# Kernel optimization log

Measured on AMD Instinct MI355X. Metric: run time of the kernel, lower is better.

## Reference

```python
import jax, jax.numpy as jnp
import numpy as np

N_NODES = 20000
N_EDGES = 640000
D = 128          # vision_dim == topo_dim
OUT = 256        # out_dim
B = 64           # image batch == num graphs
HW = 64
NEG_SLOPE = 0.2


def _sn(w2d, u):
    """PyTorch spectral_norm forward: one power iteration (u,v detached), W/sigma."""
    v = jax.lax.stop_gradient(w2d.T @ u)
    v = v / (jnp.linalg.norm(v) + 1e-12)
    u2 = jax.lax.stop_gradient(w2d @ v)
    u2 = u2 / (jnp.linalg.norm(u2) + 1e-12)
    sigma = u2 @ (w2d @ v)
    return w2d / sigma


def _leaky(x):
    return jnp.where(x >= 0, x, NEG_SLOPE * x)


def setup_inputs() -> dict:
    key = jax.random.key(0)
    ks = jax.random.split(key, 16)
    vis = jax.random.normal(ks[0], (B, D, HW, HW), dtype=jnp.float32)
    topo = jax.random.normal(ks[1], (N_NODES, D), dtype=jnp.float32)
    edge_index = jax.random.randint(ks[2], (2, N_EDGES), 0, N_NODES, dtype=jnp.int64)
    batch = jnp.sort(jax.random.randint(ks[3], (N_NODES,), 0, B, dtype=jnp.int64))
    s = 0.05
    conv_w = jax.random.normal(ks[4], (D, D, 3, 3), dtype=jnp.float32) * s
    conv_b = jnp.zeros((D,), dtype=jnp.float32)
    conv_u = jax.random.normal(ks[5], (D,), dtype=jnp.float32)
    fcv_w = jax.random.normal(ks[6], (OUT, D * 4), dtype=jnp.float32) * s
    fcv_b = jnp.zeros((OUT,), dtype=jnp.float32)
    fcv_u = jax.random.normal(ks[7], (OUT,), dtype=jnp.float32)
    gcn_w = jax.random.normal(ks[8], (D, D), dtype=jnp.float32) * s
    gcn_b = jnp.zeros((D,), dtype=jnp.float32)
    fct_w = jax.random.normal(ks[9], (OUT, D), dtype=jnp.float32) * s
    fct_b = jnp.zeros((OUT,), dtype=jnp.float32)
    fct_u = jax.random.normal(ks[10], (OUT,), dtype=jnp.float32)
    return dict(vis=vis, topo=topo, edge_index=edge_index, batch=batch,
                conv_w=conv_w, conv_b=conv_b, conv_u=conv_u,
                fcv_w=fcv_w, fcv_b=fcv_b, fcv_u=fcv_u,
                gcn_w=gcn_w, gcn_b=gcn_b,
                fct_w=fct_w, fct_b=fct_b, fct_u=fct_u)


def reference(vis, topo, edge_index, batch,
              conv_w, conv_b, conv_u,
              fcv_w, fcv_b, fcv_u,
              gcn_w, gcn_b,
              fct_w, fct_b, fct_u):
    # ---- vision head: spectral-norm conv3x3 -> leaky_relu -> adaptive max pool 2x2 -> SN linear
    cw = _sn(conv_w.reshape(D, -1), conv_u).reshape(conv_w.shape)
    x = jax.lax.conv_general_dilated(vis, cw, window_strides=(1, 1), padding='VALID',
                                     dimension_numbers=('NCHW', 'OIHW', 'NCHW'))
    x = _leaky(x + conv_b[None, :, None, None])              # [B, D, 62, 62]
    Bc, C, H, W = x.shape
    x = x.reshape(Bc, C, 2, H // 2, 2, W // 2).max(axis=(3, 5))  # adaptive max pool -> [B,D,2,2]
    x = x.reshape(Bc, -1)                                    # [B, 4D]
    vis_score = x @ _sn(fcv_w, fcv_u).T + fcv_b              # [B, OUT]

    # ---- topo head: GCNConv (sym-norm, self-loops) -> leaky_relu -> global max pool -> SN linear
    n = topo.shape[0]
    loop = jnp.arange(n, dtype=edge_index.dtype)
    src = jnp.concatenate([edge_index[0], loop])
    dst = jnp.concatenate([edge_index[1], loop])
    deg = jax.ops.segment_sum(jnp.ones_like(dst, dtype=topo.dtype), dst, num_segments=n)
    dis = jnp.where(deg > 0, jax.lax.rsqrt(jnp.maximum(deg, 1.0)), 0.0)
    norm = dis[src] * dis[dst]                               # [E+N]
    xw = topo @ gcn_w                                        # [N, D]
    h = jax.ops.segment_sum(norm[:, None] * xw[src], dst, num_segments=n) + gcn_b
    h = _leaky(h)
    pooled = jax.ops.segment_max(h, batch, num_segments=B)   # [B, D]
    topo_score = pooled @ _sn(fct_w, fct_u).T + fct_b        # [B, OUT]

    return (vis_score, topo_score)
```

## Files before the change

### kernel.cpp

```cpp
#include <hip/hip_runtime.h>
#include <hip/hip_bf16.h>
#include <float.h>
#include <stdint.h>

#define NB   64
#define CD   128
#define OUTD 256
#define NNODE 20000
#define NEDGE 640000

typedef __bf16 bf16x8 __attribute__((ext_vector_type(8)));
typedef __bf16 bf16x4 __attribute__((ext_vector_type(4)));
typedef float  f32x4  __attribute__((ext_vector_type(4)));

__device__ inline void gl_lds16(const void* g, void* l) {
  __builtin_amdgcn_global_load_lds(
      (const __attribute__((address_space(1))) void*)g,
      (__attribute__((address_space(3))) void*)l, 16, 0, 0);
}

__device__ inline void atomicMaxF(float* addr, float val) {
  if (val >= 0.f) atomicMax((int*)addr, __float_as_int(val));
  else            atomicMin((unsigned int*)addr, __float_as_uint(val));
}

__global__ void k_init(float* __restrict__ pooled_v, float* __restrict__ pooled_t,
                       int* __restrict__ cnt, int* __restrict__ fill,
                       float* __restrict__ sn_scratch, int* __restrict__ ntotal) {
  const int i = blockIdx.x * 256 + threadIdx.x;
  if (i < NB * CD * 4) pooled_v[i] = -FLT_MAX;
  if (i < NB * CD)     pooled_t[i] = -FLT_MAX;
  if (i < NNODE)       { cnt[i] = 0; fill[i] = 0; }
  if (i < 1796)        sn_scratch[i] = 0.0f;
  if (i == 0)          *ntotal = 0;
}

__global__ __launch_bounds__(256) void k_sn_v(const float* __restrict__ conv_w, const float* __restrict__ conv_u,
                                              const float* __restrict__ fcv_w,  const float* __restrict__ fcv_u,
                                              const float* __restrict__ fct_w,  const float* __restrict__ fct_u,
                                              float* __restrict__ sn) {
  const int bb = blockIdx.x;
  const float* W; const float* u; float* v; int C; int r0;
  if (bb < 16)      { W = conv_w; u = conv_u; v = sn;        C = 1152; r0 = bb * 8; }
  else if (bb < 48) { W = fcv_w;  u = fcv_u;  v = sn + 1152; C = 512;  r0 = (bb - 16) * 8; }
  else              { W = fct_w;  u = fct_u;  v = sn + 1664; C = 128;  r0 = (bb - 48) * 8; }
  const int tid = threadIdx.x;
  float acc[5] = {0.f, 0.f, 0.f, 0.f, 0.f};
  for (int i = r0; i < r0 + 8; ++i) {
    const float ui = u[i];
    const float* row = W + (size_t)i * C;
    #pragma unroll
    for (int t = 0; t < 5; ++t) {
      const int j = tid + t * 256;
      if (j < C) acc[t] += ui * row[j];
    }
  }
  #pragma unroll
  for (int t = 0; t < 5; ++t) {
    const int j = tid + t * 256;
    if (j < C) atomicAdd(&v[j], acc[t]);
  }
}

__global__ __launch_bounds__(256) void k_sn_w(const float* __restrict__ conv_w,
                                              const float* __restrict__ fcv_w,
                                              const float* __restrict__ fct_w,
                                              float* __restrict__ sn) {
  const int gw = blockIdx.x * 4 + (threadIdx.x >> 6);
  const int lane = threadIdx.x & 63;
  const float* W; const float* v; int C, m, row;
  if (gw < 128)      { W = conv_w; v = sn;        C = 1152; m = 0; row = gw; }
  else if (gw < 384) { W = fcv_w;  v = sn + 1152; C = 512;  m = 1; row = gw - 128; }
  else               { W = fct_w;  v = sn + 1664; C = 128;  m = 2; row = gw - 384; }
  const float* wr = W + (size_t)row * C;
  float y = 0.f;
  for (int c = lane; c < C; c += 64) y += wr[c] * v[c];
  #pragma unroll
  for (int s = 32; s > 0; s >>= 1) y += __shfl_xor(y, s, 64);
  if (lane == 0) atomicAdd(&sn[1792 + m], y * y);
}

__global__ __launch_bounds__(256) void k_sn_fin(const float* __restrict__ sn, float* __restrict__ inv_sigma) {
  __shared__ float red[256];
  const int tid = threadIdx.x;
  const int off[4] = {0, 1152, 1664, 1792};
  for (int m = 0; m < 3; ++m) {
    const int C = off[m + 1] - off[m];
    float ss = 0.f;
    for (int j = tid; j < C; j += 256) { const float a = sn[off[m] + j]; ss += a * a; }
    red[tid] = ss; __syncthreads();
    for (int s = 128; s > 0; s >>= 1) { if (tid < s) red[tid] += red[tid + s]; __syncthreads(); }
    if (tid == 0) inv_sigma[m] = (sqrtf(red[0]) + 1e-12f) / sqrtf(sn[1792 + m]);
    __syncthreads();
  }
}

__global__ __launch_bounds__(256, 4) void k_prep(const float* __restrict__ vis, __bf16* __restrict__ visT2,
                                                 const float* __restrict__ conv_w, const float* __restrict__ inv_sigma,
                                                 __hip_bfloat16* __restrict__ Bt2,
                                                 const int* __restrict__ dst, int* __restrict__ cnt) {
  __shared__ __bf16 tile[16384];
  const int bid = blockIdx.x;
  const int t = threadIdx.x;
  if (bid < 1024) {
    const int b = bid >> 4, y0 = (bid & 15) << 2;
    const int wave = t >> 6, lane = t & 63;
    const float* src = vis + (size_t)b * 524288 + y0 * 64 + lane * 4;
    #pragma unroll
    for (int ph = 0; ph < 2; ++ph) {
      #pragma unroll
      for (int i = 0; i < 16; ++i) {
        const int cl = wave * 16 + i;
        const int c = (ph << 6) + cl;
        const f32x4 v = *(const f32x4*)(src + (size_t)c * 4096);
        bf16x4 o;
        #pragma unroll
        for (int k = 0; k < 4; ++k) o[k] = (__bf16)v[k];
        *(bf16x4*)&tile[cl * 256 + lane * 4] = o;
      }
      __syncthreads();
      #pragma unroll
      for (int yy = 0; yy < 4; ++yy) {
        bf16x8* dstv = (bf16x8*)(visT2 + ((size_t)((b << 6) + y0 + yy) << 13)) + (ph << 9);
        #pragma unroll
        for (int k = 0; k < 2; ++k) {
          const int j = k * 256 + t;
          const int gl = j >> 6, x = j & 63;
          union { bf16x8 v; __bf16 h[8]; } u;
          #pragma unroll
          for (int cc = 0; cc < 8; ++cc)
            u.h[cc] = tile[(gl * 8 + cc) * 256 + yy * 64 + x];
          dstv[j] = u.v;
        }
      }
      if (ph == 0) __syncthreads();
    }
  } else if (bid < 1600) {
    const int tt = (bid - 1024) * 256 + t;
    if (tt < 147456) {
      const int j = tt & 7, n = (tt >> 3) & 127, s = (tt >> 10) & 7, hk = (tt >> 13) & 1, tap = tt >> 14;
      const int ci = hk * 64 + s * 8 + j;
      Bt2[tt] = __float2bfloat16(conv_w[n * 1152 + ci * 9 + tap] * inv_sigma[0]);
    }
  } else {
    const int e = (bid - 1600) * 256 + t;
    if (e < NEDGE) atomicAdd(&cnt[dst[e]], 1);
  }
}

__global__ __launch_bounds__(256, 4) void k_conv(const __hip_bfloat16* __restrict__ visT2,
                                                 const __hip_bfloat16* __restrict__ Bt2,
                                                 const float* __restrict__ conv_b,
                                                 float* __restrict__ pooled_v, int b0) {
  __shared__ bf16x8 lds_a[1024];
  __shared__ bf16x8 lds_b[1024];
  const int bx = blockIdx.x;
  const int b = b0 + bx / 31;
  const int y0 = (bx % 31) * 2;
  const int tid = threadIdx.x;
  const int wave = tid >> 6, lane = tid & 63;
  const int quad = lane >> 4, l15 = lane & 15;

  f32x4 acc[8][2];
  #pragma unroll
  for (int i = 0; i < 8; ++i) {
    acc[i][0] = f32x4{0.f, 0.f, 0.f, 0.f};
    acc[i][1] = f32x4{0.f, 0.f, 0.f, 0.f};
  }

  const __hip_bfloat16* vb = visT2 + ((size_t)b << 19);
  const int s0 = wave << 1;
  bf16x8* ldsA0 = &lds_a[s0 << 7];
  bf16x8* ldsB0 = &lds_b[s0 << 7];
  const int lane8 = lane << 3;

  for (int ky = 0; ky < 3; ++ky) {
    for (int kx = 0; kx < 3; ++kx) {
      const int tap = ky * 3 + kx;
      #pragma unroll
      for (int hk = 0; hk < 2; ++hk) {
        const __hip_bfloat16* a0p = vb + ((size_t)(((y0 + ky) << 4) + (hk << 3) + s0) << 9) + (kx << 3) + lane8;
        const __hip_bfloat16* a1p = vb + ((size_t)(((y0 + 1 + ky) << 4) + (hk << 3) + s0) << 9) + (kx << 3) + lane8;
        const __hip_bfloat16* bp  = Bt2 + (((size_t)(((tap << 1) + hk) << 3) + s0) << 10) + lane8;
        gl_lds16(a0p,        ldsA0);
        gl_lds16(a1p,        ldsA0 + 64);
        gl_lds16(a0p + 512,  ldsA0 + 128);
        gl_lds16(a1p + 512,  ldsA0 + 192);
        gl_lds16(bp,         ldsB0);
        gl_lds16(bp + 512,   ldsB0 + 64);
        gl_lds16(bp + 1024,  ldsB0 + 128);
        gl_lds16(bp + 1536,  ldsB0 + 192);
        __syncthreads();
        const bf16x8 b00 = lds_b[(quad << 7) + (wave << 5) + l15];
        const bf16x8 b01 = lds_b[(quad << 7) + (wave << 5) + 16 + l15];
        const bf16x8 b10 = lds_b[((4 + quad) << 7) + (wave << 5) + l15];
        const bf16x8 b11 = lds_b[((4 + quad) << 7) + (wave << 5) + 16 + l15];
        #pragma unroll
        for (int mt = 0; mt < 8; ++mt) {
          const bf16x8 a0 = lds_a[(quad << 7) + (mt << 4) + l15];
          const bf16x8 a1 = lds_a[((4 + quad) << 7) + (mt << 4) + l15];
          acc[mt][0] = __builtin_amdgcn_mfma_f32_16x16x32_bf16(a0, b00, acc[mt][0], 0, 0, 0);
          acc[mt][1] = __builtin_amdgcn_mfma_f32_16x16x32_bf16(a0, b01, acc[mt][1], 0, 0, 0);
          acc[mt][0] = __builtin_amdgcn_mfma_f32_16x16x32_bf16(a1, b10, acc[mt][0], 0, 0, 0);
          acc[mt][1] = __builtin_amdgcn_mfma_f32_16x16x32_bf16(a1, b11, acc[mt][1], 0, 0, 0);
        }
        __syncthreads();
      }
    }
  }

  const float cb0 = conv_b[(wave << 5) + l15];
  const float cb1 = conv_b[(wave << 5) + 16 + l15];
  float pmax[2][2][2];
  #pragma unroll
  for (int i = 0; i < 8; ++i) (&pmax[0][0][0])[i] = -FLT_MAX;

  #pragma unroll
  for (int mt = 0; mt < 8; ++mt) {
    const int py = (y0 + (mt >> 2)) >= 31 ? 1 : 0;
    #pragma unroll
    for (int r = 0; r < 4; ++r) {
      const int x = ((mt & 3) << 4) + (quad << 2) + r;
      if (x < 62) {
        const int px = x >= 31 ? 1 : 0;
        float v0 = acc[mt][0][r] + cb0;  v0 = v0 >= 0.f ? v0 : 0.2f * v0;
        float v1 = acc[mt][1][r] + cb1;  v1 = v1 >= 0.f ? v1 : 0.2f * v1;
        pmax[0][py][px] = fmaxf(pmax[0][py][px], v0);
        pmax[1][py][px] = fmaxf(pmax[1][py][px], v1);
      }
    }
  }
  #pragma unroll
  for (int nt = 0; nt < 2; ++nt)
    #pragma unroll
    for (int py = 0; py < 2; ++py)
      #pragma unroll
      for (int px = 0; px < 2; ++px) {
        float v = pmax[nt][py][px];
        v = fmaxf(v, __shfl_xor(v, 16, 64));
        v = fmaxf(v, __shfl_xor(v, 32, 64));
        if (quad == 0) {
          const int n = (wave << 5) + (nt << 4) + l15;
          atomicMaxF(&pooled_v[(size_t)b * 512 + n * 4 + py * 2 + px], v);
        }
      }
}

__global__ __launch_bounds__(256) void k_scan_xw(const int* __restrict__ cnt, int* __restrict__ offset,
                                                 int* __restrict__ total, float* __restrict__ dis,
                                                 const float* __restrict__ topo, const float* __restrict__ gcn_w,
                                                 __bf16* __restrict__ xws) {
  __shared__ f32x4 w4[4096];
  __shared__ int sbase;
  const int tid = threadIdx.x;
  if (blockIdx.x < 79) {
    int* red = (int*)w4;
    const int n = blockIdx.x * 256 + tid;
    const int v = (n < NNODE) ? cnt[n] : 0;
    red[tid] = v; __syncthreads();
    for (int d = 1; d < 256; d <<= 1) {
      const int t = (tid >= d) ? red[tid - d] : 0;
      __syncthreads();
      red[tid] += t;
      __syncthreads();
    }
    if (tid == 255) sbase = atomicAdd(total, red[255]);
    __syncthreads();
    if (n < NNODE) {
      offset[n] = sbase + red[tid] - v;
      dis[n] = rsqrtf((float)(v + 1));
    }
  } else {
    const f32x4* gw4 = (const f32x4*)gcn_w;
    for (int i = tid; i < 4096; i += 256) w4[i] = gw4[i];
    __syncthreads();
    const int n0 = (blockIdx.x - 79) * 64;
    const int jq = tid & 31, ns = tid >> 5;
    for (int pass = 0; pass < 8; ++pass) {
      const int n = n0 + pass * 8 + ns;
      if (n >= NNODE) break;
      const f32x4* tr4 = (const f32x4*)(topo + (size_t)n * 128);
      f32x4 a = {0.f, 0.f, 0.f, 0.f};
      for (int d4 = 0; d4 < 32; ++d4) {
        const f32x4 t = tr4[d4];
        const int base = (d4 << 7) + jq;
        #pragma unroll
        for (int m = 0; m < 4; ++m) {
          const f32x4 w = w4[base + m * 32];
          #pragma unroll
          for (int k = 0; k < 4; ++k) a[k] += t[m] * w[k];
        }
      }
      const float dn = rsqrtf((float)(cnt[n] + 1));
      bf16x4 o;
      #pragma unroll
      for (int k = 0; k < 4; ++k) o[k] = (__bf16)(a[k] * dn);
      ((bf16x4*)xws)[(size_t)n * 32 + jq] = o;
    }
  }
}

__global__ void k_bucket(const int* __restrict__ src, const int* __restrict__ dst,
                         const int* __restrict__ offset, int* __restrict__ fill,
                         int* __restrict__ sorted_src) {
  const int e = blockIdx.x * 256 + threadIdx.x;
  if (e >= NEDGE) return;
  const int t = dst[e];
  const int pos = atomicAdd(&fill[t], 1);
  sorted_src[offset[t] + pos] = src[e];
}

__global__ __launch_bounds__(256) void k_gather(const int* __restrict__ sorted_src,
                                                const int* __restrict__ offset, const int* __restrict__ cnt,
                                                const float* __restrict__ dis, const __bf16* __restrict__ xws,
                                                const float* __restrict__ gcn_b, const int* __restrict__ batch,
                                                float* __restrict__ pooled_t) {
  __shared__ float hred[4][128];
  __shared__ int hg[4];
  const int wave = threadIdx.x >> 6, lane = threadIdx.x & 63;
  const int n = blockIdx.x * 4 + wave;
  const int slot = lane >> 4, l16 = lane & 15;
  const int e0 = offset[n], ne = cnt[n];
  const bf16x8* x8 = (const bf16x8*)xws;
  float a[8];
  if (slot == 0) {
    const bf16x8 v = x8[(size_t)n * 16 + l16];
    #pragma unroll
    for (int k = 0; k < 8; ++k) a[k] = (float)v[k];
  } else {
    #pragma unroll
    for (int k = 0; k < 8; ++k) a[k] = 0.f;
  }
  for (int e = slot; e < ne; e += 4) {
    const int s = sorted_src[e0 + e];
    const bf16x8 v = x8[(size_t)s * 16 + l16];
    #pragma unroll
    for (int k = 0; k < 8; ++k) a[k] += (float)v[k];
  }
  #pragma unroll
  for (int k = 0; k < 8; ++k) {
    a[k] += __shfl_xor(a[k], 16, 64);
    a[k] += __shfl_xor(a[k], 32, 64);
  }
  if (lane == 0) hg[wave] = batch[n];
  if (slot == 0) {
    const float dn = dis[n];
    #pragma unroll
    for (int k = 0; k < 8; ++k) {
      float t = gcn_b[(l16 << 3) + k] + dn * a[k];
      hred[wave][(l16 << 3) + k] = t >= 0.f ? t : 0.2f * t;
    }
  }
  __syncthreads();
  const int tid = threadIdx.x;
  if (tid < 128) {
    const int g0 = hg[0], g1 = hg[1], g2 = hg[2], g3 = hg[3];
    if (g0 == g1 && g1 == g2 && g2 == g3) {
      const float m = fmaxf(fmaxf(hred[0][tid], hred[1][tid]), fmaxf(hred[2][tid], hred[3][tid]));
      atomicMaxF(&pooled_t[g0 * 128 + tid], m);
    } else {
      atomicMaxF(&pooled_t[g0 * 128 + tid], hred[0][tid]);
      atomicMaxF(&pooled_t[g1 * 128 + tid], hred[1][tid]);
      atomicMaxF(&pooled_t[g2 * 128 + tid], hred[2][tid]);
      atomicMaxF(&pooled_t[g3 * 128 + tid], hred[3][tid]);
    }
  }
}

__global__ __launch_bounds__(256) void k_fc(const float* __restrict__ pooled_v, const float* __restrict__ fcv_w,
                                            const float* __restrict__ fcv_b,
                                            const float* __restrict__ pooled_t, const float* __restrict__ fct_w,
                                            const float* __restrict__ fct_b,
                                            const float* __restrict__ inv_sigma, float* __restrict__ out) {
  const int tid = threadIdx.x;
  if (blockIdx.x < 64) {
    __shared__ f32x4 xr[128];
    const int b = blockIdx.x;
    if (tid < 128) xr[tid] = ((const f32x4*)pooled_v)[b * 128 + tid];
    __syncthreads();
    const f32x4* wr = (const f32x4*)(fcv_w + (size_t)tid * 512);
    f32x4 a4 = {0.f, 0.f, 0.f, 0.f};
    for (int f = 0; f < 128; ++f) {
      const f32x4 x = xr[f];
      const f32x4 w = wr[f];
      #pragma unroll
      for (int k = 0; k < 4; ++k) a4[k] += x[k] * w[k];
    }
    const float a = a4[0] + a4[1] + a4[2] + a4[3];
    out[b * 256 + tid] = a * inv_sigma[1] + fcv_b[tid];
  } else {
    __shared__ f32x4 xr2[32];
    const int b = blockIdx.x - 64;
    if (tid < 32) xr2[tid] = ((const f32x4*)pooled_t)[b * 32 + tid];
    __syncthreads();
    const f32x4* wr = (const f32x4*)(fct_w + (size_t)tid * 128);
    f32x4 a4 = {0.f, 0.f, 0.f, 0.f};
    for (int f = 0; f < 32; ++f) {
      const f32x4 x = xr2[f];
      const f32x4 w = wr[f];
      #pragma unroll
      for (int k = 0; k < 4; ++k) a4[k] += x[k] * w[k];
    }
    const float a = a4[0] + a4[1] + a4[2] + a4[3];
    out[NB * 256 + b * 256 + tid] = a * inv_sigma[2] + fct_b[tid];
  }
}

extern "C" void kernel_launch(void* const* d_in, const int* in_sizes, int n_in,
                              void* d_out, int out_size, void* d_ws, size_t ws_size,
                              hipStream_t stream) {
  const float* vis    = (const float*)d_in[0];
  const float* topo   = (const float*)d_in[1];
  const int*   eidx   = (const int*)d_in[2];
  const int*   batch  = (const int*)d_in[3];
  const float* conv_w = (const float*)d_in[4];
  const float* conv_b = (const float*)d_in[5];
  const float* conv_u = (const float*)d_in[6];
  const float* fcv_w  = (const float*)d_in[7];
  const float* fcv_b  = (const float*)d_in[8];
  const float* fcv_u  = (const float*)d_in[9];
  const float* gcn_w  = (const float*)d_in[10];
  const float* gcn_b  = (const float*)d_in[11];
  const float* fct_w  = (const float*)d_in[12];
  const float* fct_b  = (const float*)d_in[13];
  const float* fct_u  = (const float*)d_in[14];
  float* out = (float*)d_out;

  char* p = (char*)d_ws;
  float* inv_sigma  = (float*)p; p += 256;
  float* sn_scratch = (float*)p; p += 1796 * 4 + 240;
  float* pooled_v   = (float*)p; p += (size_t)NB * 512 * 4;
  float* pooled_t   = (float*)p; p += (size_t)NB * 128 * 4;
  int*   cnt        = (int*)p;   p += (size_t)NNODE * 4;
  int*   offset     = (int*)p;   p += (size_t)NNODE * 4;
  int*   fill       = (int*)p;   p += (size_t)NNODE * 4;
  float* dis        = (float*)p; p += (size_t)NNODE * 4;
  int*   ntotal     = (int*)p;   p += 256;
  int*   sorted_src = (int*)p;   p += (size_t)NEDGE * 4;
  __bf16* xws       = (__bf16*)p; p += (size_t)NNODE * 128 * 2 + 256;
  __hip_bfloat16* Bt2 = (__hip_bfloat16*)p; p += (size_t)147456 * 2;
  p = (char*)(((uintptr_t)p + 255) & ~(uintptr_t)255);
  __bf16* visT2 = (__bf16*)p;

  hipLaunchKernelGGL(k_init,    dim3(128),  dim3(256), 0, stream, pooled_v, pooled_t, cnt, fill, sn_scratch, ntotal);
  hipLaunchKernelGGL(k_sn_v,    dim3(80),   dim3(256), 0, stream, conv_w, conv_u, fcv_w, fcv_u, fct_w, fct_u, sn_scratch);
  hipLaunchKernelGGL(k_sn_w,    dim3(160),  dim3(256), 0, stream, conv_w, fcv_w, fct_w, sn_scratch);
  hipLaunchKernelGGL(k_sn_fin,  dim3(1),    dim3(256), 0, stream, sn_scratch, inv_sigma);
  hipLaunchKernelGGL(k_prep,    dim3(4100), dim3(256), 0, stream, vis, visT2, conv_w, inv_sigma, Bt2, eidx + NEDGE, cnt);
  hipLaunchKernelGGL(k_scan_xw, dim3(392),  dim3(256), 0, stream, cnt, offset, ntotal, dis, topo, gcn_w, xws);
  hipLaunchKernelGGL(k_conv,    dim3(32*31), dim3(256), 0, stream, (const __hip_bfloat16*)visT2, Bt2, conv_b, pooled_v, 0);
  hipLaunchKernelGGL(k_conv,    dim3(32*31), dim3(256), 0, stream, (const __hip_bfloat16*)visT2, Bt2, conv_b, pooled_v, 32);
  hipLaunchKernelGGL(k_bucket,  dim3(2500), dim3(256), 0, stream, eidx, eidx + NEDGE, offset, fill, sorted_src);
  hipLaunchKernelGGL(k_gather,  dim3(5000), dim3(256), 0, stream, sorted_src, offset, cnt, dis, xws, gcn_b, batch, pooled_t);
  hipLaunchKernelGGL(k_fc,      dim3(128),  dim3(256), 0, stream, pooled_v, fcv_w, fcv_b, pooled_t, fct_w, fct_b, inv_sigma, out);
}
```

Before: 485.1 us.

## Fuse launch chain into fewer multi-role kernels and merge conv launches

Reduces the launch sequence from eleven kernels to seven. Init, spectral-norm v computation and the vis transpose are merged into one front kernel. The sn row norms and the edge degree count share a kernel, and the sigma finalisation moves into the scan kernel. Weight packing is combined with edge bucketing, and the two conv launches are merged into one grid over all 64 images. Spectral-norm atomics are replaced by direct per-column and per-row writes to scratch. The aim is to cut launch gaps and serial tiny kernels, at the cost of more block-role branching and reordered dependencies between stages.

```diff
diff --git a/kernel.cpp b/kernel.cpp
--- a/kernel.cpp
+++ b/kernel.cpp
@@ -24,86 +24,39 @@
   else            atomicMin((unsigned int*)addr, __float_as_uint(val));
 }
 
-__global__ void k_init(float* __restrict__ pooled_v, float* __restrict__ pooled_t,
-                       int* __restrict__ cnt, int* __restrict__ fill,
-                       float* __restrict__ sn_scratch, int* __restrict__ ntotal) {
-  const int i = blockIdx.x * 256 + threadIdx.x;
-  if (i < NB * CD * 4) pooled_v[i] = -FLT_MAX;
-  if (i < NB * CD)     pooled_t[i] = -FLT_MAX;
-  if (i < NNODE)       { cnt[i] = 0; fill[i] = 0; }
-  if (i < 1796)        sn_scratch[i] = 0.0f;
-  if (i == 0)          *ntotal = 0;
-}
-
-__global__ __launch_bounds__(256) void k_sn_v(const float* __restrict__ conv_w, const float* __restrict__ conv_u,
-                                              const float* __restrict__ fcv_w,  const float* __restrict__ fcv_u,
-                                              const float* __restrict__ fct_w,  const float* __restrict__ fct_u,
-                                              float* __restrict__ sn) {
-  const int bb = blockIdx.x;
-  const float* W; const float* u; float* v; int C; int r0;
-  if (bb < 16)      { W = conv_w; u = conv_u; v = sn;        C = 1152; r0 = bb * 8; }
-  else if (bb < 48) { W = fcv_w;  u = fcv_u;  v = sn + 1152; C = 512;  r0 = (bb - 16) * 8; }
-  else              { W = fct_w;  u = fct_u;  v = sn + 1664; C = 128;  r0 = (bb - 48) * 8; }
-  const int tid = threadIdx.x;
-  float acc[5] = {0.f, 0.f, 0.f, 0.f, 0.f};
-  for (int i = r0; i < r0 + 8; ++i) {
-    const float ui = u[i];
-    const float* row = W + (size_t)i * C;
-    #pragma unroll
-    for (int t = 0; t < 5; ++t) {
-      const int j = tid + t * 256;
-      if (j < C) acc[t] += ui * row[j];
-    }
-  }
-  #pragma unroll
-  for (int t = 0; t < 5; ++t) {
-    const int j = tid + t * 256;
-    if (j < C) atomicAdd(&v[j], acc[t]);
-  }
-}
-
-__global__ __launch_bounds__(256) void k_sn_w(const float* __restrict__ conv_w,
-                                              const float* __restrict__ fcv_w,
-                                              const float* __restrict__ fct_w,
-                                              float* __restrict__ sn) {
-  const int gw = blockIdx.x * 4 + (threadIdx.x >> 6);
-  const int lane = threadIdx.x & 63;
-  const float* W; const float* v; int C, m, row;
-  if (gw < 128)      { W = conv_w; v = sn;        C = 1152; m = 0; row = gw; }
-  else if (gw < 384) { W = fcv_w;  v = sn + 1152; C = 512;  m = 1; row = gw - 128; }
-  else               { W = fct_w;  v = sn + 1664; C = 128;  m = 2; row = gw - 384; }
-  const float* wr = W + (size_t)row * C;
-  float y = 0.f;
-  for (int c = lane; c < C; c += 64) y += wr[c] * v[c];
-  #pragma unroll
-  for (int s = 32; s > 0; s >>= 1) y += __shfl_xor(y, s, 64);
-  if (lane == 0) atomicAdd(&sn[1792 + m], y * y);
-}
-
-__global__ __launch_bounds__(256) void k_sn_fin(const float* __restrict__ sn, float* __restrict__ inv_sigma) {
-  __shared__ float red[256];
-  const int tid = threadIdx.x;
-  const int off[4] = {0, 1152, 1664, 1792};
-  for (int m = 0; m < 3; ++m) {
-    const int C = off[m + 1] - off[m];
-    float ss = 0.f;
-    for (int j = tid; j < C; j += 256) { const float a = sn[off[m] + j]; ss += a * a; }
-    red[tid] = ss; __syncthreads();
-    for (int s = 128; s > 0; s >>= 1) { if (tid < s) red[tid] += red[tid + s]; __syncthreads(); }
-    if (tid == 0) inv_sigma[m] = (sqrtf(red[0]) + 1e-12f) / sqrtf(sn[1792 + m]);
-    __syncthreads();
-  }
-}
-
-__global__ __launch_bounds__(256, 4) void k_prep(const float* __restrict__ vis, __bf16* __restrict__ visT2,
-                                                 const float* __restrict__ conv_w, const float* __restrict__ inv_sigma,
-                                                 __hip_bfloat16* __restrict__ Bt2,
-                                                 const int* __restrict__ dst, int* __restrict__ cnt) {
+
+__global__ __launch_bounds__(256, 4) void k_front(float* __restrict__ pooled_v, float* __restrict__ pooled_t,
+                                                  int* __restrict__ cnt, int* __restrict__ fill,
+                                                  int* __restrict__ ntotal,
+                                                  const float* __restrict__ conv_w, const float* __restrict__ conv_u,
+                                                  const float* __restrict__ fcv_w,  const float* __restrict__ fcv_u,
+                                                  const float* __restrict__ fct_w,  const float* __restrict__ fct_u,
+                                                  float* __restrict__ sn,
+                                                  const float* __restrict__ vis, __bf16* __restrict__ visT2) {
   __shared__ __bf16 tile[16384];
   const int bid = blockIdx.x;
   const int t = threadIdx.x;
-  if (bid < 1024) {
-    const int b = bid >> 4, y0 = (bid & 15) << 2;
+  if (bid < 128) {
+    const int i = bid * 256 + t;
+    if (i < NB * CD * 4) pooled_v[i] = -FLT_MAX;
+    if (i < NB * CD)     pooled_t[i] = -FLT_MAX;
+    if (i < NNODE)       { cnt[i] = 0; fill[i] = 0; }
+    if (i == 0)          *ntotal = 0;
+  } else if (bid < 136) {
+    const int bb = bid - 128;
+    const float* W; const float* u; float* v; int C, R, c0;
+    if (bb < 5)      { W = conv_w; u = conv_u; v = sn;        C = 1152; R = 128; c0 = bb * 256; }
+    else if (bb < 7) { W = fcv_w;  u = fcv_u;  v = sn + 1152; C = 512;  R = 256; c0 = (bb - 5) * 256; }
+    else             { W = fct_w;  u = fct_u;  v = sn + 1664; C = 128;  R = 256; c0 = 0; }
+    const int col = c0 + t;
+    if (col < C) {
+      float acc = 0.f;
+      for (int i = 0; i < R; ++i) acc += u[i] * W[(size_t)i * C + col];
+      v[col] = acc;
+    }
+  } else {
+    const int bb = bid - 136;
+    const int b = bb >> 4, y0 = (bb & 15) << 2;
     const int wave = t >> 6, lane = t & 63;
     const float* src = vis + (size_t)b * 524288 + y0 * 64 + lane * 4;
     #pragma unroll
@@ -135,27 +88,139 @@
       }
       if (ph == 0) __syncthreads();
     }
-  } else if (bid < 1600) {
-    const int tt = (bid - 1024) * 256 + t;
-    if (tt < 147456) {
-      const int j = tt & 7, n = (tt >> 3) & 127, s = (tt >> 10) & 7, hk = (tt >> 13) & 1, tap = tt >> 14;
-      const int ci = hk * 64 + s * 8 + j;
-      Bt2[tt] = __float2bfloat16(conv_w[n * 1152 + ci * 9 + tap] * inv_sigma[0]);
-    }
-  } else {
-    const int e = (bid - 1600) * 256 + t;
-    if (e < NEDGE) atomicAdd(&cnt[dst[e]], 1);
+  }
+}
+
+__global__ __launch_bounds__(256) void k_mid(const float* __restrict__ conv_w,
+                                             const float* __restrict__ fcv_w,
+                                             const float* __restrict__ fct_w,
+                                             float* __restrict__ sn,
+                                             const int* __restrict__ dstE, int* __restrict__ cnt) {
+  const int bid = blockIdx.x;
+  if (bid < 160) {
+    const int gw = bid * 4 + (threadIdx.x >> 6);
+    const int lane = threadIdx.x & 63;
+    const float* W; const float* v; int C, row;
+    if (gw < 128)      { W = conv_w; v = sn;        C = 1152; row = gw; }
+    else if (gw < 384) { W = fcv_w;  v = sn + 1152; C = 512;  row = gw - 128; }
+    else               { W = fct_w;  v = sn + 1664; C = 128;  row = gw - 384; }
+    const float* wr = W + (size_t)row * C;
+    float y = 0.f;
+    for (int c = lane; c < C; c += 64) y += wr[c] * v[c];
+    #pragma unroll
+    for (int s = 32; s > 0; s >>= 1) y += __shfl_xor(y, s, 64);
+    if (lane == 0) sn[1800 + gw] = y * y;
+  } else {
+    const int e = (bid - 160) * 256 + threadIdx.x;
+    if (e < NEDGE) atomicAdd(&cnt[dstE[e]], 1);
+  }
+}
+
+__global__ __launch_bounds__(256) void k_scan_xw(const int* __restrict__ cnt, int* __restrict__ offset,
+                                                 int* __restrict__ total, float* __restrict__ dis,
+                                                 const float* __restrict__ topo, const float* __restrict__ gcn_w,
+                                                 __bf16* __restrict__ xws,
+                                                 float* __restrict__ sn, float* __restrict__ inv_sigma) {
+  __shared__ f32x4 w4[4096];
+  __shared__ int sbase;
+  const int tid = threadIdx.x;
+  const int bid = blockIdx.x;
+  if (bid == 0) {
+    float* red = (float*)w4;
+    const int offv[3] = {0, 1152, 1664};
+    const int Cv[3]   = {1152, 512, 128};
+    const int offp[3] = {1800, 1928, 2184};
+    const int Cp[3]   = {128, 256, 256};
+    for (int m = 0; m < 3; ++m) {
+      float s1 = 0.f;
+      for (int j = tid; j < Cv[m]; j += 256) { const float a = sn[offv[m] + j]; s1 += a * a; }
+      red[tid] = s1; __syncthreads();
+      for (int s = 128; s > 0; s >>= 1) { if (tid < s) red[tid] += red[tid + s]; __syncthreads(); }
+      const float v2 = red[0]; __syncthreads();
+      float s2 = 0.f;
+      for (int j = tid; j < Cp[m]; j += 256) s2 += sn[offp[m] + j];
+      red[tid] = s2; __syncthreads();
+      for (int s = 128; s > 0; s >>= 1) { if (tid < s) red[tid] += red[tid + s]; __syncthreads(); }
+      if (tid == 0) inv_sigma[m] = (sqrtf(v2) + 1e-12f) / sqrtf(red[0]);
+      __syncthreads();
+    }
+  } else if (bid < 80) {
+    int* red = (int*)w4;
+    const int n = (bid - 1) * 256 + tid;
+    const int v = (n < NNODE) ? cnt[n] : 0;
+    red[tid] = v; __syncthreads();
+    for (int d = 1; d < 256; d <<= 1) {
+      const int t = (tid >= d) ? red[tid - d] : 0;
+      __syncthreads();
+      red[tid] += t;
+      __syncthreads();
+    }
+    if (tid == 255) sbase = atomicAdd(total, red[255]);
+    __syncthreads();
+    if (n < NNODE) {
+      offset[n] = sbase + red[tid] - v;
+      dis[n] = rsqrtf((float)(v + 1));
+    }
+  } else {
+    const f32x4* gw4 = (const f32x4*)gcn_w;
+    for (int i = tid; i < 4096; i += 256) w4[i] = gw4[i];
+    __syncthreads();
+    const int n0 = (bid - 80) * 64;
+    const int jq = tid & 31, ns = tid >> 5;
+    for (int pass = 0; pass < 8; ++pass) {
+      const int n = n0 + pass * 8 + ns;
+      if (n >= NNODE) break;
+      const f32x4* tr4 = (const f32x4*)(topo + (size_t)n * 128);
+      f32x4 a = {0.f, 0.f, 0.f, 0.f};
+      for (int d4 = 0; d4 < 32; ++d4) {
+        const f32x4 t = tr4[d4];
+        const int base = (d4 << 7) + jq;
+        #pragma unroll
+        for (int m = 0; m < 4; ++m) {
+          const f32x4 w = w4[base + m * 32];
+          #pragma unroll
+          for (int k = 0; k < 4; ++k) a[k] += t[m] * w[k];
+        }
+      }
+      const float dn = rsqrtf((float)(cnt[n] + 1));
+      bf16x4 o;
+      #pragma unroll
+      for (int k = 0; k < 4; ++k) o[k] = (__bf16)(a[k] * dn);
+      ((bf16x4*)xws)[(size_t)n * 32 + jq] = o;
+    }
+  }
+}
+
+__global__ void k_pack_bucket(const float* __restrict__ conv_w, const float* __restrict__ inv_sigma,
+                              __hip_bfloat16* __restrict__ Bt2,
+                              const int* __restrict__ srcE, const int* __restrict__ dstE,
+                              const int* __restrict__ offset, int* __restrict__ fill,
+                              int* __restrict__ sorted_src) {
+  const int bid = blockIdx.x;
+  const int t = threadIdx.x;
+  if (bid < 576) {
+    const int tt = bid * 256 + t;
+    const int j = tt & 7, n = (tt >> 3) & 127, s = (tt >> 10) & 7, hk = (tt >> 13) & 1, tap = tt >> 14;
+    const int ci = hk * 64 + s * 8 + j;
+    Bt2[tt] = __float2bfloat16(conv_w[n * 1152 + ci * 9 + tap] * inv_sigma[0]);
+  } else {
+    const int e = (bid - 576) * 256 + t;
+    if (e < NEDGE) {
+      const int tt = dstE[e];
+      const int pos = atomicAdd(&fill[tt], 1);
+      sorted_src[offset[tt] + pos] = srcE[e];
+    }
   }
 }
 
 __global__ __launch_bounds__(256, 4) void k_conv(const __hip_bfloat16* __restrict__ visT2,
                                                  const __hip_bfloat16* __restrict__ Bt2,
                                                  const float* __restrict__ conv_b,
-                                                 float* __restrict__ pooled_v, int b0) {
+                                                 float* __restrict__ pooled_v) {
   __shared__ bf16x8 lds_a[1024];
   __shared__ bf16x8 lds_b[1024];
   const int bx = blockIdx.x;
-  const int b = b0 + bx / 31;
+  const int b = bx / 31;
   const int y0 = (bx % 31) * 2;
   const int tid = threadIdx.x;
   const int wave = tid >> 6, lane = tid & 63;
@@ -246,70 +311,6 @@
       }
 }
 
-__global__ __launch_bounds__(256) void k_scan_xw(const int* __restrict__ cnt, int* __restrict__ offset,
-                                                 int* __restrict__ total, float* __restrict__ dis,
-                                                 const float* __restrict__ topo, const float* __restrict__ gcn_w,
-                                                 __bf16* __restrict__ xws) {
-  __shared__ f32x4 w4[4096];
-  __shared__ int sbase;
-  const int tid = threadIdx.x;
-  if (blockIdx.x < 79) {
-    int* red = (int*)w4;
-    const int n = blockIdx.x * 256 + tid;
-    const int v = (n < NNODE) ? cnt[n] : 0;
-    red[tid] = v; __syncthreads();
-    for (int d = 1; d < 256; d <<= 1) {
-      const int t = (tid >= d) ? red[tid - d] : 0;
-      __syncthreads();
-      red[tid] += t;
-      __syncthreads();
-    }
-    if (tid == 255) sbase = atomicAdd(total, red[255]);
-    __syncthreads();
-    if (n < NNODE) {
-      offset[n] = sbase + red[tid] - v;
-      dis[n] = rsqrtf((float)(v + 1));
-    }
-  } else {
-    const f32x4* gw4 = (const f32x4*)gcn_w;
-    for (int i = tid; i < 4096; i += 256) w4[i] = gw4[i];
-    __syncthreads();
-    const int n0 = (blockIdx.x - 79) * 64;
-    const int jq = tid & 31, ns = tid >> 5;
-    for (int pass = 0; pass < 8; ++pass) {
-      const int n = n0 + pass * 8 + ns;
-      if (n >= NNODE) break;
-      const f32x4* tr4 = (const f32x4*)(topo + (size_t)n * 128);
-      f32x4 a = {0.f, 0.f, 0.f, 0.f};
-      for (int d4 = 0; d4 < 32; ++d4) {
-        const f32x4 t = tr4[d4];
-        const int base = (d4 << 7) + jq;
-        #pragma unroll
-        for (int m = 0; m < 4; ++m) {
-          const f32x4 w = w4[base + m * 32];
-          #pragma unroll
-          for (int k = 0; k < 4; ++k) a[k] += t[m] * w[k];
-        }
-      }
-      const float dn = rsqrtf((float)(cnt[n] + 1));
-      bf16x4 o;
-      #pragma unroll
-      for (int k = 0; k < 4; ++k) o[k] = (__bf16)(a[k] * dn);
-      ((bf16x4*)xws)[(size_t)n * 32 + jq] = o;
-    }
-  }
-}
-
-__global__ void k_bucket(const int* __restrict__ src, const int* __restrict__ dst,
-                         const int* __restrict__ offset, int* __restrict__ fill,
-                         int* __restrict__ sorted_src) {
-  const int e = blockIdx.x * 256 + threadIdx.x;
-  if (e >= NEDGE) return;
-  const int t = dst[e];
-  const int pos = atomicAdd(&fill[t], 1);
-  sorted_src[offset[t] + pos] = src[e];
-}
-
 __global__ __launch_bounds__(256) void k_gather(const int* __restrict__ sorted_src,
                                                 const int* __restrict__ offset, const int* __restrict__ cnt,
                                                 const float* __restrict__ dis, const __bf16* __restrict__ xws,
@@ -428,7 +429,7 @@
 
   char* p = (char*)d_ws;
   float* inv_sigma  = (float*)p; p += 256;
-  float* sn_scratch = (float*)p; p += 1796 * 4 + 240;
+  float* sn_scratch = (float*)p; p += 2560 * 4;
   float* pooled_v   = (float*)p; p += (size_t)NB * 512 * 4;
   float* pooled_t   = (float*)p; p += (size_t)NB * 128 * 4;
   int*   cnt        = (int*)p;   p += (size_t)NNODE * 4;
@@ -442,15 +443,19 @@
   p = (char*)(((uintptr_t)p + 255) & ~(uintptr_t)255);
   __bf16* visT2 = (__bf16*)p;
 
-  hipLaunchKernelGGL(k_init,    dim3(128),  dim3(256), 0, stream, pooled_v, pooled_t, cnt, fill, sn_scratch, ntotal);
-  hipLaunchKernelGGL(k_sn_v,    dim3(80),   dim3(256), 0, stream, conv_w, conv_u, fcv_w, fcv_u, fct_w, fct_u, sn_scratch);
-  hipLaunchKernelGGL(k_sn_w,    dim3(160),  dim3(256), 0, stream, conv_w, fcv_w, fct_w, sn_scratch);
-  hipLaunchKernelGGL(k_sn_fin,  dim3(1),    dim3(256), 0, stream, sn_scratch, inv_sigma);
-  hipLaunchKernelGGL(k_prep,    dim3(4100), dim3(256), 0, stream, vis, visT2, conv_w, inv_sigma, Bt2, eidx + NEDGE, cnt);
-  hipLaunchKernelGGL(k_scan_xw, dim3(392),  dim3(256), 0, stream, cnt, offset, ntotal, dis, topo, gcn_w, xws);
-  hipLaunchKernelGGL(k_conv,    dim3(32*31), dim3(256), 0, stream, (const __hip_bfloat16*)visT2, Bt2, conv_b, pooled_v, 0);
-  hipLaunchKernelGGL(k_conv,    dim3(32*31), dim3(256), 0, stream, (const __hip_bfloat16*)visT2, Bt2, conv_b, pooled_v, 32);
-  hipLaunchKernelGGL(k_bucket,  dim3(2500), dim3(256), 0, stream, eidx, eidx + NEDGE, offset, fill, sorted_src);
-  hipLaunchKernelGGL(k_gather,  dim3(5000), dim3(256), 0, stream, sorted_src, offset, cnt, dis, xws, gcn_b, batch, pooled_t);
-  hipLaunchKernelGGL(k_fc,      dim3(128),  dim3(256), 0, stream, pooled_v, fcv_w, fcv_b, pooled_t, fct_w, fct_b, inv_sigma, out);
-}
+  hipLaunchKernelGGL(k_front, dim3(1160), dim3(256), 0, stream,
+                     pooled_v, pooled_t, cnt, fill, ntotal,
+                     conv_w, conv_u, fcv_w, fcv_u, fct_w, fct_u, sn_scratch, vis, visT2);
+  hipLaunchKernelGGL(k_mid, dim3(2660), dim3(256), 0, stream,
+                     conv_w, fcv_w, fct_w, sn_scratch, eidx + NEDGE, cnt);
+  hipLaunchKernelGGL(k_scan_xw, dim3(393), dim3(256), 0, stream,
+                     cnt, offset, ntotal, dis, topo, gcn_w, xws, sn_scratch, inv_sigma);
+  hipLaunchKernelGGL(k_pack_bucket, dim3(3076), dim3(256), 0, stream,
+                     conv_w, inv_sigma, Bt2, eidx, eidx + NEDGE, offset, fill, sorted_src);
+  hipLaunchKernelGGL(k_conv, dim3(64 * 31), dim3(256), 0, stream,
+                     (const __hip_bfloat16*)visT2, Bt2, conv_b, pooled_v);
+  hipLaunchKernelGGL(k_gather, dim3(5000), dim3(256), 0, stream,
+                     sorted_src, offset, cnt, dis, xws, gcn_b, batch, pooled_t);
+  hipLaunchKernelGGL(k_fc, dim3(128), dim3(256), 0, stream,
+                     pooled_v, fcv_w, fcv_b, pooled_t, fct_w, fct_b, inv_sigma, out);
+}
```

After: 541.7 us. 11.6% more time.
